# Performance work log

Hardware: AMD Instinct MI355X
Metric: run time of the kernel (lower is better)

Reference implementation:

```python
import jax, jax.numpy as jnp
import numpy as np

EPS = 1e-08


def _norm(H, add):
    # Faithful to GTN.norm: transpose, mask/set diagonal, row-normalize by degree, transpose back.
    # The original O(N^3) mm(deg_inv_diag, H) is expressed as an O(N^2) row scaling (same math).
    Ht = H.T
    n = Ht.shape[0]
    eye = jnp.eye(n, dtype=H.dtype)
    Ht = Ht * (1.0 - eye)
    if add:
        Ht = Ht + eye
    deg = jnp.sum(Ht, axis=1)
    deg_inv = jnp.where(deg == 0, 0.0, 1.0 / (deg + EPS))
    return (deg_inv[:, None] * Ht).T


def _gtconv(A, w):
    # A: [E, N, N]; w: [C, E, 1, 1] -> softmax over E, weighted sum of adjacency channels.
    s = jax.nn.softmax(w[:, :, 0, 0], axis=1)  # [C, E]
    return jnp.einsum('ce,eij->cij', s, A)     # [C, N, N]


def setup_inputs() -> dict:
    key = jax.random.key(0)
    k = jax.random.split(key, 6)
    E, N, C, w_in, w_out = 5, 2048, 2, 256, 64
    A = jax.random.uniform(k[0], (E, N, N), dtype=jnp.float32)
    X = jax.random.normal(k[1], (N, w_in), dtype=jnp.float32)
    conv_w_l0_1 = jax.random.normal(k[2], (C, E, 1, 1), dtype=jnp.float32)
    conv_w_l0_2 = jax.random.normal(k[3], (C, E, 1, 1), dtype=jnp.float32)
    conv_w_l1 = jax.random.normal(k[4], (C, E, 1, 1), dtype=jnp.float32)
    gcn_weight = jax.random.normal(k[5], (w_in, w_out), dtype=jnp.float32) * (1.0 / np.sqrt(w_in))
    return {"A": A, "X": X, "conv_w_l0_1": conv_w_l0_1, "conv_w_l0_2": conv_w_l0_2,
            "conv_w_l1": conv_w_l1, "gcn_weight": gcn_weight}


def reference(A, X, conv_w_l0_1, conv_w_l0_2, conv_w_l1, gcn_weight):
    N = A.shape[1]
    # Layer 0 (first=True): two GTConvs, meta-path composition via bmm.
    a = _gtconv(A, conv_w_l0_1)            # [C, N, N]
    b = _gtconv(A, conv_w_l0_2)            # [C, N, N]
    H = jnp.einsum('cij,cjk->cik', a, b)   # [C, N, N]
    # Layer 1 (first=False): normalize per channel, then compose with new conv.
    H = jax.vmap(lambda h: _norm(h, False))(H)
    a1 = _gtconv(A, conv_w_l1)
    H = jnp.einsum('cij,cjk->cik', H, a1)
    # GCN readout per channel: mm(norm_add(H_c).T, X @ W), relu, concat along features.
    Xw = X @ gcn_weight                     # [N, w_out]
    Hn = jax.vmap(lambda h: _norm(h, True))(H)   # [C, N, N]
    Xc = jax.nn.relu(jnp.einsum('cji,jk->cik', Hn, Xw))  # [C, N, w_out]
    X_ = jnp.transpose(Xc, (1, 0, 2)).reshape(N, -1)     # [N, C*w_out]
    return X_
```

## Files before the change

### kernel.cpp

```cpp
#include <hip/hip_runtime.h>
#include <cstdint>
#include <cstddef>

typedef unsigned short u16;
typedef __attribute__((ext_vector_type(8))) short short8;
typedef __attribute__((ext_vector_type(4))) float v4f;

static constexpr size_t NN = (size_t)2048 * 2048;
#define N2 2048

typedef __attribute__((address_space(1))) const unsigned int guint;
typedef __attribute__((address_space(3))) unsigned int luint;

__device__ __forceinline__ float b2f_bits(uint32_t hi) { union { uint32_t u; float f; } v; v.u = hi; return v.f; }
__device__ __forceinline__ float b2f(u16 x) { return b2f_bits((uint32_t)x << 16); }
__device__ __forceinline__ u16 f2b(float f) {
  union { float f; uint32_t u; } v; v.f = f;
  uint32_t r = v.u + 0x7fffu + ((v.u >> 16) & 1u);
  return (u16)(r >> 16);
}
__device__ __forceinline__ uint4 pack8(const float* f) {
  uint4 u;
  u.x = (uint32_t)f2b(f[0]) | ((uint32_t)f2b(f[1]) << 16);
  u.y = (uint32_t)f2b(f[2]) | ((uint32_t)f2b(f[3]) << 16);
  u.z = (uint32_t)f2b(f[4]) | ((uint32_t)f2b(f[5]) << 16);
  u.w = (uint32_t)f2b(f[6]) | ((uint32_t)f2b(f[7]) << 16);
  return u;
}
__device__ __forceinline__ float sgprf(float x) {
  union { float f; int i; } v; v.f = x;
  v.i = __builtin_amdgcn_readfirstlane(v.i);
  return v.f;
}

__global__ __launch_bounds__(512, 2) void conv_kernel(
    const float* __restrict__ A, const float* __restrict__ w1,
    const float* __restrict__ w2, const float* __restrict__ w3,
    const float* __restrict__ X, const float* __restrict__ W,
    u16* __restrict__ abf, u16* __restrict__ bbt, u16* __restrict__ a1t,
    u16* __restrict__ a1r, u16* __restrict__ Xwt,
    float* __restrict__ zeroZT, int* __restrict__ counters)
{
  __shared__ u16 LT[2][64 * 64];
  const int t = threadIdx.x;
  const int bid = (int)(blockIdx.y * 32 + blockIdx.x);
  const int i0 = blockIdx.y * 64, j0 = blockIdx.x * 64;
  const int m = t >> 3;
  const int cg = t & 7;
  const int n0 = cg * 8;

  zeroZT[(size_t)bid * 512 + t] = 0.f;
  if (bid == 0 && t < 64) counters[t] = 0;

  float sc[3][2][5];
  {
    const float* wsrc[3] = { w1, w2, w3 };
    for (int q = 0; q < 3; ++q)
      for (int c = 0; c < 2; ++c) {
        float v[5], mx = -1e30f, sum = 0.f;
        #pragma unroll
        for (int e = 0; e < 5; ++e) { v[e] = wsrc[q][c * 5 + e]; mx = fmaxf(mx, v[e]); }
        #pragma unroll
        for (int e = 0; e < 5; ++e) { v[e] = expf(v[e] - mx); sum += v[e]; }
        #pragma unroll
        for (int e = 0; e < 5; ++e) sc[q][c][e] = sgprf(v[e] / sum);
      }
  }

  float av[2][8], bv[2][8], cv[2][8];
  #pragma unroll
  for (int c = 0; c < 2; ++c)
    #pragma unroll
    for (int u = 0; u < 8; ++u) { av[c][u] = 0.f; bv[c][u] = 0.f; cv[c][u] = 0.f; }

  #pragma unroll
  for (int e = 0; e < 5; ++e) {
    const float* base = A + (size_t)e * NN + (size_t)(i0 + m) * N2 + (j0 + n0);
    float4 x0 = ((const float4*)base)[0];
    float4 x1 = ((const float4*)base)[1];
    float f[8] = { x0.x, x0.y, x0.z, x0.w, x1.x, x1.y, x1.z, x1.w };
    #pragma unroll
    for (int c = 0; c < 2; ++c)
      #pragma unroll
      for (int u = 0; u < 8; ++u) {
        av[c][u] += sc[0][c][e] * f[u];
        bv[c][u] += sc[1][c][e] * f[u];
        cv[c][u] += sc[2][c][e] * f[u];
      }
  }

  #pragma unroll
  for (int c = 0; c < 2; ++c) {
    *(uint4*)(abf + (size_t)c * NN + (size_t)(i0 + m) * N2 + (j0 + n0)) = pack8(av[c]);
    *(uint4*)(a1r + (size_t)c * NN + (size_t)(i0 + m) * N2 + (j0 + n0)) = pack8(cv[c]);
  }
  const int swb = ((m >> 3) ^ cg) & 7;
  const int mlo = m & 7;
  const int on = t >> 3;
  const int mb = t & 7;
  const int src = on * 64 + (((mb ^ (on >> 3)) & 7) * 8);
  #pragma unroll
  for (int c = 0; c < 2; ++c) {
    if (c == 1) __syncthreads();
    #pragma unroll
    for (int u = 0; u < 8; ++u) {
      const int idx = (n0 + u) * 64 + swb * 8 + mlo;
      LT[0][idx] = f2b(bv[c][u]);
      LT[1][idx] = f2b(cv[c][u]);
    }
    __syncthreads();
    *(uint4*)(bbt + (size_t)c * NN + (size_t)(j0 + on) * N2 + (i0 + mb * 8)) =
        *(const uint4*)&LT[0][src];
    *(uint4*)(a1t + (size_t)c * NN + (size_t)(j0 + on) * N2 + (i0 + mb * 8)) =
        *(const uint4*)&LT[1][src];
  }
  if (t < 128) {
    const int n = bid * 2 + (t >> 6);
    const int k = t & 63;
    float acc = 0.f;
    for (int mm = 0; mm < 256; ++mm)
      acc += X[n * 256 + mm] * W[mm * 64 + k];
    Xwt[(size_t)k * N2 + n] = f2b(acc);
  }
}

__global__ __launch_bounds__(256, 3) void gemm_kernel(
    const u16* __restrict__ Ain, const u16* __restrict__ Btin,
    u16* __restrict__ Cout, float* __restrict__ csp, float* __restrict__ diag)
{
  const int c = blockIdx.z;
  const u16* Ac = Ain + (size_t)c * NN;
  const u16* Bc = Btin + (size_t)c * NN;
  const int m0 = blockIdx.y * 128, n0 = blockIdx.x * 128;
  const int t = threadIdx.x, w = t >> 6, lane = t & 63;
  const int quad = lane >> 4, r = lane & 15;
  __shared__ u16 SM[128 * 64 + 128 * 64];
  u16* As = SM;
  u16* Bs = SM + 128 * 64;

  v4f zero4 = { 0.f, 0.f, 0.f, 0.f };
  v4f acc[2][8];
  #pragma unroll
  for (int i = 0; i < 2; ++i)
    #pragma unroll
    for (int j = 0; j < 8; ++j) acc[i][j] = zero4;

  const int srow = lane >> 3;
  const int sgran = (lane & 7) ^ srow;

  for (int kt = 0; kt < 2048; kt += 64) {
    __syncthreads();
    #pragma unroll
    for (int i = 0; i < 4; ++i) {
      const int chunk = i * 4 + w;
      const u16* ga = Ac + (size_t)(m0 + chunk * 8 + srow) * N2 + kt + sgran * 8;
      __builtin_amdgcn_global_load_lds((guint*)ga, (luint*)(As + chunk * 512), 16, 0, 0);
    }
    #pragma unroll
    for (int i = 0; i < 4; ++i) {
      const int chunk = i * 4 + w;
      const u16* gb = Bc + (size_t)(n0 + chunk * 8 + srow) * N2 + kt + sgran * 8;
      __builtin_amdgcn_global_load_lds((guint*)gb, (luint*)(Bs + chunk * 512), 16, 0, 0);
    }
    __syncthreads();
    #pragma unroll
    for (int ks = 0; ks < 2; ++ks) {
      const int sl = ((ks * 4 + quad) ^ (r & 7)) * 8;
      short8 af[2], bf[8];
      #pragma unroll
      for (int i = 0; i < 2; ++i)
        af[i] = *(const short8*)(As + (w * 32 + i * 16 + r) * 64 + sl);
      #pragma unroll
      for (int j = 0; j < 8; ++j)
        bf[j] = *(const short8*)(Bs + (j * 16 + r) * 64 + sl);
      #pragma unroll
      for (int i = 0; i < 2; ++i)
        #pragma unroll
        for (int j = 0; j < 8; ++j)
          acc[i][j] = __builtin_amdgcn_mfma_f32_16x16x32_bf16(af[i], bf[j], acc[i][j], 0, 0, 0);
    }
  }
  if (blockIdx.x == blockIdx.y) {
    #pragma unroll
    for (int i = 0; i < 2; ++i) {
      const int rowg = m0 + w * 32 + i * 16 + quad * 4;
      #pragma unroll
      for (int j = 0; j < 8; ++j) {
        const int colg = n0 + j * 16 + r;
        #pragma unroll
        for (int g = 0; g < 4; ++g)
          if (rowg + g == colg) diag[c * N2 + colg] = acc[i][j][g];
      }
    }
  }
  float s[8];
  #pragma unroll
  for (int j = 0; j < 8; ++j) {
    s[j] = 0.f;
    #pragma unroll
    for (int i = 0; i < 2; ++i)
      #pragma unroll
      for (int g = 0; g < 4; ++g) s[j] += acc[i][j][g];
    s[j] += __shfl_xor(s[j], 16);
    s[j] += __shfl_xor(s[j], 32);
  }
  __syncthreads();
  float* csl = (float*)SM;
  if (quad == 0) {
    #pragma unroll
    for (int j = 0; j < 8; ++j) csl[w * 128 + j * 16 + r] = s[j];
  }
  __syncthreads();
  if (t < 128) {
    const float v = csl[t] + csl[128 + t] + csl[256 + t] + csl[384 + t];
    csp[((size_t)(c * 16) + blockIdx.y) * N2 + n0 + t] = v;
  }
  {
    u16* tb = SM;
    u16* Cc = Cout + (size_t)c * NN;
    #pragma unroll
    for (int h = 0; h < 2; ++h) {
      __syncthreads();
      #pragma unroll
      for (int i = 0; i < 2; ++i) {
        #pragma unroll
        for (int jl = 0; jl < 4; ++jl) {
          const int j = h * 4 + jl;
          #pragma unroll
          for (int g = 0; g < 4; ++g)
            tb[(jl * 16 + r) * 136 + (w * 32 + i * 16 + quad * 4 + g)] = f2b(acc[i][j][g]);
        }
      }
      __syncthreads();
      const int rown = t >> 2, seg = t & 3;
      const u16* ps = tb + rown * 136 + seg * 32;
      uint4* pd = (uint4*)(Cc + (size_t)(n0 + h * 64 + rown) * N2 + m0 + seg * 32);
      pd[0] = ((const uint4*)ps)[0];
      pd[1] = ((const uint4*)ps)[1];
      pd[2] = ((const uint4*)ps)[2];
      pd[3] = ((const uint4*)ps)[3];
    }
  }
}

__global__ __launch_bounds__(256) void zgemm_kernel(
    const u16* __restrict__ Ht, const u16* __restrict__ Xwt,
    const u16* __restrict__ a1r, const float* __restrict__ csp,
    const float* __restrict__ diag1, float* __restrict__ Z,
    float* __restrict__ dp, float* __restrict__ cp)
{
  const int c = blockIdx.z, split = blockIdx.y, mt = blockIdx.x;
  const int m0 = mt * 128;
  const u16* Ac = Ht + (size_t)c * NN;
  const int t = threadIdx.x, w = t >> 6, lane = t & 63;
  const int quad = lane >> 4, r = lane & 15;
  __shared__ u16 SMZ[128 * 64 + 64 * 64];
  u16* As = SMZ;
  u16* Bs = SMZ + 128 * 64;

  v4f zero4 = { 0.f, 0.f, 0.f, 0.f };
  v4f acc[2][4];
  #pragma unroll
  for (int i = 0; i < 2; ++i)
    #pragma unroll
    for (int j = 0; j < 4; ++j) acc[i][j] = zero4;

  const int srow = lane >> 3;
  const int sgran = (lane & 7) ^ srow;

  for (int kk = 0; kk < 4; ++kk) {
    const int kt = split * 256 + kk * 64;
    __syncthreads();
    #pragma unroll
    for (int i = 0; i < 4; ++i) {
      const int chunk = i * 4 + w;
      const u16* ga = Ac + (size_t)(m0 + chunk * 8 + srow) * N2 + kt + sgran * 8;
      __builtin_amdgcn_global_load_lds((guint*)ga, (luint*)(As + chunk * 512), 16, 0, 0);
    }
    #pragma unroll
    for (int i = 0; i < 2; ++i) {
      const int chunk = i * 4 + w;
      const u16* gb = Xwt + (size_t)(chunk * 8 + srow) * N2 + kt + sgran * 8;
      __builtin_amdgcn_global_load_lds((guint*)gb, (luint*)(Bs + chunk * 512), 16, 0, 0);
    }
    __syncthreads();
    #pragma unroll
    for (int ks = 0; ks < 2; ++ks) {
      const int sl = ((ks * 4 + quad) ^ (r & 7)) * 8;
      short8 af[2], bf[4];
      #pragma unroll
      for (int i = 0; i < 2; ++i)
        af[i] = *(const short8*)(As + (w * 32 + i * 16 + r) * 64 + sl);
      #pragma unroll
      for (int j = 0; j < 4; ++j)
        bf[j] = *(const short8*)(Bs + (j * 16 + r) * 64 + sl);
      #pragma unroll
      for (int i = 0; i < 2; ++i)
        #pragma unroll
        for (int j = 0; j < 4; ++j)
          acc[i][j] = __builtin_amdgcn_mfma_f32_16x16x32_bf16(af[i], bf[j], acc[i][j], 0, 0, 0);
    }
  }
  #pragma unroll
  for (int i = 0; i < 2; ++i) {
    const int rowg = m0 + w * 32 + i * 16 + quad * 4;
    #pragma unroll
    for (int j = 0; j < 4; ++j) {
      const int colg = j * 16 + r;
      float* base = Z + (size_t)(c * 64 + colg) * N2 + rowg;
      #pragma unroll
      for (int g = 0; g < 4; ++g)
        atomicAdd(base + g, acc[i][j][g]);
    }
  }
  __syncthreads();
  float* ci_l = (float*)SMZ;
  float* wv_l = ci_l + 128;
  if (t < 128) {
    const int i = m0 + t;
    float cs = 0.f;
    #pragma unroll
    for (int s = 0; s < 16; ++s) cs += csp[((size_t)(c * 16) + s) * N2 + i];
    const float deg = cs - diag1[c * N2 + i];
    const float v = (deg == 0.f) ? 0.f : 1.f / (deg + 1e-8f);
    ci_l[t] = v;
    wv_l[t] = v * deg;
  }
  __syncthreads();
  const int j4 = (t & 15) * 4, ig = t >> 4;
  float dacc[4][4], cacc[4][4];
  #pragma unroll
  for (int kk = 0; kk < 4; ++kk) {
    const int gj = split * 256 + kk * 64 + j4;
    #pragma unroll
    for (int u = 0; u < 4; ++u) { dacc[kk][u] = 0.f; cacc[kk][u] = 0.f; }
    for (int ii = 0; ii < 8; ++ii) {
      const int i = m0 + ig * 8 + ii;
      uint2 hu = *(const uint2*)(Ht  + (size_t)c * NN + (size_t)i * N2 + gj);
      uint2 au = *(const uint2*)(a1r + (size_t)c * NN + (size_t)i * N2 + gj);
      float h[4], a[4];
      h[0] = b2f_bits(hu.x << 16); h[1] = b2f_bits(hu.x & 0xffff0000u);
      h[2] = b2f_bits(hu.y << 16); h[3] = b2f_bits(hu.y & 0xffff0000u);
      a[0] = b2f_bits(au.x << 16); a[1] = b2f_bits(au.x & 0xffff0000u);
      a[2] = b2f_bits(au.y << 16); a[3] = b2f_bits(au.y & 0xffff0000u);
      const float cq = ci_l[ig * 8 + ii];
      const float wq = wv_l[ig * 8 + ii];
      #pragma unroll
      for (int u = 0; u < 4; ++u) {
        cacc[kk][u] += wq * a[u];
        const float tv = cq * h[u] * a[u];
        dacc[kk][u] += (i == gj + u) ? 0.f : tv;
      }
    }
  }
  float* red = ci_l + 256;
  __syncthreads();
  #pragma unroll
  for (int kk = 0; kk < 4; ++kk)
    #pragma unroll
    for (int u = 0; u < 4; ++u) red[ig * 256 + kk * 64 + j4 + u] = dacc[kk][u];
  __syncthreads();
  {
    float v = 0.f;
    #pragma unroll
    for (int g = 0; g < 16; ++g) v += red[g * 256 + t];
    dp[((size_t)(c * 16) + mt) * N2 + split * 256 + t] = v;
  }
  __syncthreads();
  #pragma unroll
  for (int kk = 0; kk < 4; ++kk)
    #pragma unroll
    for (int u = 0; u < 4; ++u) red[ig * 256 + kk * 64 + j4 + u] = cacc[kk][u];
  __syncthreads();
  {
    float v = 0.f;
    #pragma unroll
    for (int g = 0; g < 16; ++g) v += red[g * 256 + t];
    cp[((size_t)(c * 16) + mt) * N2 + split * 256 + t] = v;
  }
}

__global__ __launch_bounds__(256) void tgemm_kernel(
    const u16* __restrict__ a1t, const float* __restrict__ csp,
    const float* __restrict__ diag1, const float* __restrict__ Z,
    const u16* __restrict__ Xwt, const float* __restrict__ dp,
    const float* __restrict__ cp, float* __restrict__ T,
    float* __restrict__ out, int* __restrict__ counters)
{
  const int c = blockIdx.z, split = blockIdx.y, mt = blockIdx.x;
  const int m0 = mt * 128, kt0 = split * 256;
  const int t = threadIdx.x, w = t >> 6, lane = t & 63;
  const int quad = lane >> 4, r = lane & 15;
  __shared__ u16 As[128 * 64];
  __shared__ u16 Bp[64 * 256];
  __shared__ float cif[256], d1f[256];

  {
    const int jj = kt0 + t;
    float cs = 0.f;
    #pragma unroll
    for (int s = 0; s < 16; ++s) cs += csp[((size_t)(c * 16) + s) * N2 + jj];
    const float d1 = diag1[c * N2 + jj];
    const float deg = cs - d1;
    cif[t] = (deg == 0.f) ? 0.f : 1.f / (deg + 1e-8f);
    d1f[t] = d1;
  }
  __syncthreads();
  {
    const int kk = t >> 6, g = (t >> 3) & 7, el = t & 7;
    const float civ = cif[t], d1v = d1f[t];
    const float* zcol = Z + (size_t)(c * 64) * N2 + kt0 + t;
    const u16* xcol = Xwt + kt0 + t;
    for (int k = 0; k < 64; ++k) {
      const float z = zcol[(size_t)k * N2];
      const float xw = b2f(xcol[(size_t)k * N2]);
      Bp[k * 256 + kk * 64 + ((g ^ (k & 7)) * 8) + el] = f2b(civ * (z - d1v * xw));
    }
  }

  v4f zero4 = { 0.f, 0.f, 0.f, 0.f };
  v4f acc[2][4];
  #pragma unroll
  for (int i = 0; i < 2; ++i)
    #pragma unroll
    for (int j = 0; j < 4; ++j) acc[i][j] = zero4;

  const int srow = lane >> 3;
  const int sgran = (lane & 7) ^ srow;

  for (int kk = 0; kk < 4; ++kk) {
    const int kt = kt0 + kk * 64;
    __syncthreads();
    #pragma unroll
    for (int i = 0; i < 4; ++i) {
      const int chunk = i * 4 + w;
      const u16* ga = a1t + (size_t)c * NN + (size_t)(m0 + chunk * 8 + srow) * N2 + kt + sgran * 8;
      __builtin_amdgcn_global_load_lds((guint*)ga, (luint*)(As + chunk * 512), 16, 0, 0);
    }
    __syncthreads();
    #pragma unroll
    for (int ks = 0; ks < 2; ++ks) {
      const int sl = ((ks * 4 + quad) ^ (r & 7)) * 8;
      short8 af[2], bf[4];
      #pragma unroll
      for (int i = 0; i < 2; ++i)
        af[i] = *(const short8*)(As + (w * 32 + i * 16 + r) * 64 + sl);
      #pragma unroll
      for (int j = 0; j < 4; ++j)
        bf[j] = *(const short8*)(Bp + (j * 16 + r) * 256 + kk * 64 + sl);
      #pragma unroll
      for (int i = 0; i < 2; ++i)
        #pragma unroll
        for (int j = 0; j < 4; ++j)
          acc[i][j] = __builtin_amdgcn_mfma_f32_16x16x32_bf16(af[i], bf[j], acc[i][j], 0, 0, 0);
    }
  }
  #pragma unroll
  for (int i = 0; i < 2; ++i) {
    const int rowg = m0 + w * 32 + i * 16 + quad * 4;
    #pragma unroll
    for (int j = 0; j < 4; ++j) {
      const int colg = j * 16 + r;
      float* base = T + ((size_t)(c * 2048) + rowg) * 64 + colg;
      #pragma unroll
      for (int g = 0; g < 4; ++g)
        atomicAdd(base + (size_t)g * 64, acc[i][j][g]);
    }
  }
  __shared__ int eLast;
  __syncthreads();
  if (t == 0) {
    __threadfence();
    eLast = (atomicAdd(&counters[mt * 2 + c], 1) == 7);
  }
  __syncthreads();
  if (eLast) {
    __threadfence();
    const int i = m0 + (t >> 1), kh = (t & 1) * 32;
    float ds = 0.f, cs = 0.f;
    #pragma unroll
    for (int b = 0; b < 16; ++b) {
      ds += dp[((size_t)(c * 16) + b) * N2 + i];
      cs += cp[((size_t)(c * 16) + b) * N2 + i];
    }
    const float deg = cs - ds + 1.0f;
    const float dv = (deg == 0.f) ? 0.f : 1.f / (deg + 1e-8f);
    #pragma unroll
    for (int k2 = 0; k2 < 32; ++k2) {
      const int k = kh + k2;
      const float Tv = T[((size_t)(c * 2048) + i) * 64 + k];
      const float xw = b2f(Xwt[(size_t)k * N2 + i]);
      float v = dv * (Tv - ds * xw + xw);
      v = v > 0.f ? v : 0.f;
      out[(size_t)i * 128 + c * 64 + k] = v;
    }
  }
}

extern "C" void kernel_launch(void* const* d_in, const int* in_sizes, int n_in,
                              void* d_out, int out_size, void* d_ws, size_t ws_size,
                              hipStream_t stream) {
  const float* A  = (const float*)d_in[0];
  const float* X  = (const float*)d_in[1];
  const float* w1 = (const float*)d_in[2];
  const float* w2 = (const float*)d_in[3];
  const float* w3 = (const float*)d_in[4];
  const float* W  = (const float*)d_in[5];
  float* out = (float*)d_out;
  char* ws = (char*)d_ws;

  u16*   abf   = (u16*)(ws + 0);
  u16*   bbt   = (u16*)(ws + 16777216);
  u16*   a1t   = (u16*)(ws + 33554432);
  u16*   a1r   = (u16*)(ws + 50331648);
  u16*   Ht    = (u16*)(ws + 67108864);
  u16*   Xwt   = (u16*)(ws + 83886080);
  float* cspa  = (float*)(ws + 84148224);
  float* diag1 = (float*)(ws + 84410368);
  float* dp    = (float*)(ws + 84426752);
  float* cp    = (float*)(ws + 84688896);
  float* Z     = (float*)(ws + 84951040);
  float* T     = (float*)(ws + 85999616);
  int*   cnt   = (int*)  (ws + 87048192);

  conv_kernel<<<dim3(32, 32), 512, 0, stream>>>(A, w1, w2, w3, X, W, abf, bbt, a1t, a1r, Xwt, Z, cnt);
  gemm_kernel<<<dim3(16, 16, 2), 256, 0, stream>>>(abf, bbt, Ht, cspa, diag1);
  zgemm_kernel<<<dim3(16, 8, 2), 256, 0, stream>>>(Ht, Xwt, a1r, cspa, diag1, Z, dp, cp);
  tgemm_kernel<<<dim3(16, 8, 2), 256, 0, stream>>>(a1t, cspa, diag1, Z, Xwt, dp, cp, T, out, cnt);
}
```

Before: 262.3 us.

## Double split-K parallelism in zgemm/tgemm and spread Xw computation across blocks

```diff
diff --git a/kernel.cpp b/kernel.cpp
--- a/kernel.cpp
+++ b/kernel.cpp
@@ -114,13 +114,16 @@
     *(uint4*)(a1t + (size_t)c * NN + (size_t)(j0 + on) * N2 + (i0 + mb * 8)) =
         *(const uint4*)&LT[1][src];
   }
-  if (t < 128) {
-    const int n = bid * 2 + (t >> 6);
-    const int k = t & 63;
+  if (blockIdx.y < 16) {
+    const int pair = t >> 1, half = t & 1;
+    const int n = (int)(blockIdx.y * 32 + blockIdx.x) * 4 + (pair >> 6);
+    const int k = pair & 63;
     float acc = 0.f;
-    for (int mm = 0; mm < 256; ++mm)
+    const int mmb = half * 128;
+    for (int mm = mmb; mm < mmb + 128; ++mm)
       acc += X[n * 256 + mm] * W[mm * 64 + k];
-    Xwt[(size_t)k * N2 + n] = f2b(acc);
+    acc += __shfl_xor(acc, 1);
+    if (half == 0) Xwt[(size_t)k * N2 + n] = f2b(acc);
   }
 }
 
@@ -243,7 +246,7 @@
   }
 }
 
-__global__ __launch_bounds__(256) void zgemm_kernel(
+__global__ __launch_bounds__(256, 4) void zgemm_kernel(
     const u16* __restrict__ Ht, const u16* __restrict__ Xwt,
     const u16* __restrict__ a1r, const float* __restrict__ csp,
     const float* __restrict__ diag1, float* __restrict__ Z,
@@ -268,8 +271,9 @@
   const int srow = lane >> 3;
   const int sgran = (lane & 7) ^ srow;
 
-  for (int kk = 0; kk < 4; ++kk) {
-    const int kt = split * 256 + kk * 64;
+  #pragma unroll
+  for (int kk = 0; kk < 2; ++kk) {
+    const int kt = split * 128 + kk * 64;
     __syncthreads();
     #pragma unroll
     for (int i = 0; i < 4; ++i) {
@@ -328,10 +332,10 @@
   }
   __syncthreads();
   const int j4 = (t & 15) * 4, ig = t >> 4;
-  float dacc[4][4], cacc[4][4];
-  #pragma unroll
-  for (int kk = 0; kk < 4; ++kk) {
-    const int gj = split * 256 + kk * 64 + j4;
+  float dacc[2][4], cacc[2][4];
+  #pragma unroll
+  for (int kk = 0; kk < 2; ++kk) {
+    const int gj = split * 128 + kk * 64 + j4;
     #pragma unroll
     for (int u = 0; u < 4; ++u) { dacc[kk][u] = 0.f; cacc[kk][u] = 0.f; }
     for (int ii = 0; ii < 8; ++ii) {
@@ -356,31 +360,25 @@
   float* red = ci_l + 256;
   __syncthreads();
   #pragma unroll
-  for (int kk = 0; kk < 4; ++kk)
-    #pragma unroll
-    for (int u = 0; u < 4; ++u) red[ig * 256 + kk * 64 + j4 + u] = dacc[kk][u];
+  for (int kk = 0; kk < 2; ++kk)
+    #pragma unroll
+    for (int u = 0; u < 4; ++u) {
+      red[ig * 256 + kk * 64 + j4 + u] = dacc[kk][u];
+      red[ig * 256 + 128 + kk * 64 + j4 + u] = cacc[kk][u];
+    }
   __syncthreads();
   {
     float v = 0.f;
     #pragma unroll
     for (int g = 0; g < 16; ++g) v += red[g * 256 + t];
-    dp[((size_t)(c * 16) + mt) * N2 + split * 256 + t] = v;
-  }
-  __syncthreads();
-  #pragma unroll
-  for (int kk = 0; kk < 4; ++kk)
-    #pragma unroll
-    for (int u = 0; u < 4; ++u) red[ig * 256 + kk * 64 + j4 + u] = cacc[kk][u];
-  __syncthreads();
-  {
-    float v = 0.f;
-    #pragma unroll
-    for (int g = 0; g < 16; ++g) v += red[g * 256 + t];
-    cp[((size_t)(c * 16) + mt) * N2 + split * 256 + t] = v;
-  }
-}
-
-__global__ __launch_bounds__(256) void tgemm_kernel(
+    if (t < 128)
+      dp[((size_t)(c * 16) + mt) * N2 + split * 128 + t] = v;
+    else
+      cp[((size_t)(c * 16) + mt) * N2 + split * 128 + (t - 128)] = v;
+  }
+}
+
+__global__ __launch_bounds__(256, 4) void tgemm_kernel(
     const u16* __restrict__ a1t, const float* __restrict__ csp,
     const float* __restrict__ diag1, const float* __restrict__ Z,
     const u16* __restrict__ Xwt, const float* __restrict__ dp,
@@ -388,33 +386,35 @@
     float* __restrict__ out, int* __restrict__ counters)
 {
   const int c = blockIdx.z, split = blockIdx.y, mt = blockIdx.x;
-  const int m0 = mt * 128, kt0 = split * 256;
+  const int m0 = mt * 128, kt0 = split * 128;
   const int t = threadIdx.x, w = t >> 6, lane = t & 63;
   const int quad = lane >> 4, r = lane & 15;
   __shared__ u16 As[128 * 64];
-  __shared__ u16 Bp[64 * 256];
-  __shared__ float cif[256], d1f[256];
-
-  {
-    const int jj = kt0 + t;
+  __shared__ u16 Bp[64 * 128];
+  __shared__ float cif[128], d1f[128];
+
+  const int jl = t & 127;
+  if (t < 128) {
+    const int jj = kt0 + jl;
     float cs = 0.f;
     #pragma unroll
     for (int s = 0; s < 16; ++s) cs += csp[((size_t)(c * 16) + s) * N2 + jj];
     const float d1 = diag1[c * N2 + jj];
     const float deg = cs - d1;
-    cif[t] = (deg == 0.f) ? 0.f : 1.f / (deg + 1e-8f);
-    d1f[t] = d1;
+    cif[jl] = (deg == 0.f) ? 0.f : 1.f / (deg + 1e-8f);
+    d1f[jl] = d1;
   }
   __syncthreads();
   {
-    const int kk = t >> 6, g = (t >> 3) & 7, el = t & 7;
-    const float civ = cif[t], d1v = d1f[t];
-    const float* zcol = Z + (size_t)(c * 64) * N2 + kt0 + t;
-    const u16* xcol = Xwt + kt0 + t;
-    for (int k = 0; k < 64; ++k) {
+    const int kkc = jl >> 6, g = (jl >> 3) & 7, el = jl & 7;
+    const int kh = (t >> 7) * 32;
+    const float civ = cif[jl], d1v = d1f[jl];
+    const float* zcol = Z + (size_t)(c * 64) * N2 + kt0 + jl;
+    const u16* xcol = Xwt + kt0 + jl;
+    for (int k = kh; k < kh + 32; ++k) {
       const float z = zcol[(size_t)k * N2];
       const float xw = b2f(xcol[(size_t)k * N2]);
-      Bp[k * 256 + kk * 64 + ((g ^ (k & 7)) * 8) + el] = f2b(civ * (z - d1v * xw));
+      Bp[k * 128 + kkc * 64 + ((g ^ (k & 7)) * 8) + el] = f2b(civ * (z - d1v * xw));
     }
   }
 
@@ -428,7 +428,8 @@
   const int srow = lane >> 3;
   const int sgran = (lane & 7) ^ srow;
 
-  for (int kk = 0; kk < 4; ++kk) {
+  #pragma unroll
+  for (int kk = 0; kk < 2; ++kk) {
     const int kt = kt0 + kk * 64;
     __syncthreads();
     #pragma unroll
@@ -447,7 +448,7 @@
         af[i] = *(const short8*)(As + (w * 32 + i * 16 + r) * 64 + sl);
       #pragma unroll
       for (int j = 0; j < 4; ++j)
-        bf[j] = *(const short8*)(Bp + (j * 16 + r) * 256 + kk * 64 + sl);
+        bf[j] = *(const short8*)(Bp + (j * 16 + r) * 128 + kk * 64 + sl);
       #pragma unroll
       for (int i = 0; i < 2; ++i)
         #pragma unroll
@@ -471,7 +472,7 @@
   __syncthreads();
   if (t == 0) {
     __threadfence();
-    eLast = (atomicAdd(&counters[mt * 2 + c], 1) == 7);
+    eLast = (atomicAdd(&counters[mt * 2 + c], 1) == 15);
   }
   __syncthreads();
   if (eLast) {
@@ -525,6 +526,6 @@
 
   conv_kernel<<<dim3(32, 32), 512, 0, stream>>>(A, w1, w2, w3, X, W, abf, bbt, a1t, a1r, Xwt, Z, cnt);
   gemm_kernel<<<dim3(16, 16, 2), 256, 0, stream>>>(abf, bbt, Ht, cspa, diag1);
-  zgemm_kernel<<<dim3(16, 8, 2), 256, 0, stream>>>(Ht, Xwt, a1r, cspa, diag1, Z, dp, cp);
-  tgemm_kernel<<<dim3(16, 8, 2), 256, 0, stream>>>(a1t, cspa, diag1, Z, Xwt, dp, cp, T, out, cnt);
-}
+  zgemm_kernel<<<dim3(16, 16, 2), 256, 0, stream>>>(Ht, Xwt, a1r, cspa, diag1, Z, dp, cp);
+  tgemm_kernel<<<dim3(16, 16, 2), 256, 0, stream>>>(a1t, cspa, diag1, Z, Xwt, dp, cp, T, out, cnt);
+}
```

After: 300.4 us. 1.15x slower.
